# Kernel tuning notes

Measured on AMD Instinct MI355X. Metric: run time of the kernel, lower is better.

The kernel has to match this reference:

```python
import jax, jax.numpy as jnp
import numpy as np

B, L, D = 16, 2048, 128


def setup_inputs() -> dict:
    key = jax.random.key(0)
    k1, k2 = jax.random.split(key)
    x = jax.random.normal(k1, (B, L, D), dtype=jnp.float32)
    mask = jax.random.uniform(k2, (B, L), dtype=jnp.float32)
    return {"input": x, "mask": mask}


def reference(input, mask):
    # mask broadcast over feature dim (torch: mask.unsqueeze(-1).repeat(1,1,D))
    x = input * mask[:, :, None]                       # [B, L, D]
    # attn_weights = bmm(x, x^T) -> [B, L, L]
    scores = jnp.einsum('bld,bmd->blm', x, x)
    # softmax over dim=1 (the FIRST L axis, i.e. columns normalized over rows)
    w = jax.nn.softmax(scores, axis=1)                 # [B, L, L]
    # out = bmm(w^T, x).mean(dim=1, keepdim=True): out_full[b,m,d] = sum_l w[b,l,m] * x[b,l,d]
    out = jnp.einsum('blm,bld->bmd', w, x).mean(axis=1, keepdims=True)  # [B, 1, D]
    attn_mean = w.mean(axis=1)                         # [B, L]
    return (out, attn_mean)
```

## Files before the change

### kernel.cpp

```cpp
#include <hip/hip_runtime.h>
#include <math.h>


constexpr int NB = 16, NL = 2048, ND = 128;
constexpr int ROWS_US = 128;
constexpr int NSLOT = 20;

typedef __attribute__((ext_vector_type(8))) short short8;
typedef __attribute__((ext_vector_type(4))) float f32x4;

#define EXP2(x) __builtin_amdgcn_exp2f(x)

__device__ __forceinline__ unsigned short f2bf(float f) {
  unsigned u = __builtin_bit_cast(unsigned, f);
  u += 0x7FFFu + ((u >> 16) & 1u);
  return (unsigned short)(u >> 16);
}
__device__ __forceinline__ float bf2f(unsigned short h) {
  unsigned u = ((unsigned)h) << 16;
  return __builtin_bit_cast(float, u);
}

__device__ __forceinline__ void stage16(const unsigned short* g, unsigned short* l) {
  __builtin_amdgcn_global_load_lds(
      (const __attribute__((address_space(1))) unsigned int*)g,
      (__attribute__((address_space(3))) unsigned int*)l, 16, 0, 0);
}

__global__ __launch_bounds__(256) void k_prep(const float* __restrict__ x,
                                              const float* __restrict__ mask,
                                              unsigned short* __restrict__ Y,
                                              float* __restrict__ nsq) {
  const int gid = blockIdx.x * 256 + threadIdx.x;
  const int row = gid >> 5;
  const int dq = gid & 31;
  const float4 v = reinterpret_cast<const float4*>(x)[gid];
  const float m = mask[row] * 1.2011224087864498f;
  const unsigned short h0 = f2bf(v.x * m), h1 = f2bf(v.y * m),
                       h2 = f2bf(v.z * m), h3 = f2bf(v.w * m);
  const float g0 = bf2f(h0), g1 = bf2f(h1), g2 = bf2f(h2), g3 = bf2f(h3);
  unsigned short* Yr = Y + (size_t)row * ROWS_US;
  const int sx = dq >> 1, half8 = (dq & 1) * 4;
  const int pos = sx ^ (row & 15);
  *reinterpret_cast<ushort4*>(Yr + pos * 8 + half8) = make_ushort4(h0, h1, h2, h3);
  float ss = g0 * g0 + g1 * g1 + g2 * g2 + g3 * g3;
#pragma unroll
  for (int mk = 1; mk < 32; mk <<= 1) ss += __shfl_xor(ss, mk);
  if (dq == 0) nsq[row] = ss;
}

__global__ __launch_bounds__(256) void k_nmax(const float* __restrict__ nsq,
                                              float* __restrict__ nmax) {
  const int b = blockIdx.x;
  const int tid = threadIdx.x;
  float m = 0.f;
  for (int i = tid; i < NL; i += 256) m = fmaxf(m, nsq[b * NL + i]);
#pragma unroll
  for (int mk = 1; mk < 64; mk <<= 1) m = fmaxf(m, __shfl_xor(m, mk));
  __shared__ float red[4];
  if ((tid & 63) == 0) red[tid >> 6] = m;
  __syncthreads();
  if (tid == 0) nmax[b] = fmaxf(fmaxf(red[0], red[1]), fmaxf(red[2], red[3]));
}

#define STRIP_DECODE()                                     \
  const int sid = blockIdx.x;                              \
  const int idx = sid >> 3;                                \
  const int b = ((sid & 7) << 1) | (idx >> 5);             \
  const int strip = idx & 31;                              \
  const int ib = strip >> 1, hf = strip & 1;               \
  const int d0 = hf * 4;                                   \
  const int nt = (hf == 0) ? 4 : ((ib < 8) ? 5 : 4);       \
  const int row0 = ib * 128;                               \
  const int tid = threadIdx.x;                             \
  const int lane = tid & 63, wave = tid >> 6;              \
  const int wr = wave >> 1, wc = wave & 1;                 \
  const int lhi = lane >> 4, llo = lane & 15;

#define STAGE_AT(dst, Yb, r0)                                               \
  _Pragma("unroll") for (int it = 0; it < 8; ++it) {                        \
    const int idx2 = tid + 256 * it;                                        \
    const int r = idx2 >> 4, s = idx2 & 15;                                 \
    stage16((Yb) + (size_t)((r0) + r) * ROWS_US + s * 8, (dst) + idx2 * 8); \
  }

#define STAGE_BH(dst, Yb, c0)                                               \
  _Pragma("unroll") for (int it = 0; it < 4; ++it) {                        \
    const int idx2 = tid + 256 * it;                                        \
    const int r = idx2 >> 4, s = idx2 & 15;                                 \
    stage16((Yb) + (size_t)((c0) + r) * ROWS_US + s * 8, (dst) + idx2 * 8); \
  }

#define HALF_MFMA(Atp, Btp)                                                  \
  f32x4 acc[4][2];                                                           \
  _Pragma("unroll") for (int rs = 0; rs < 4; ++rs)                           \
      _Pragma("unroll") for (int cs = 0; cs < 2; ++cs)                       \
          acc[rs][cs] = f32x4{0.f, 0.f, 0.f, 0.f};                           \
  _Pragma("unroll") for (int t4 = 0; t4 < 4; ++t4) {                         \
    const int sl = 4 * t4 + lhi;                                             \
    short8 af[4], bf[2];                                                     \
    _Pragma("unroll") for (int qq = 0; qq < 4; ++qq) {                       \
      const int ra = 64 * wr + 16 * qq + llo;                                \
      af[qq] = *(const short8*)((Atp) + ra * 128 + ((sl ^ (ra & 15)) << 3)); \
    }                                                                        \
    _Pragma("unroll") for (int cs = 0; cs < 2; ++cs) {                       \
      const int rb = 32 * wc + 16 * cs + llo;                                \
      bf[cs] = *(const short8*)((Btp) + rb * 128 + ((sl ^ (rb & 15)) << 3)); \
    }                                                                        \
    _Pragma("unroll") for (int rs = 0; rs < 4; ++rs)                         \
        _Pragma("unroll") for (int cs = 0; cs < 2; ++cs)                     \
            acc[rs][cs] = __builtin_amdgcn_mfma_f32_16x16x32_bf16(           \
                af[rs], bf[cs], acc[rs][cs], 0, 0, 0);                       \
  }

__global__ __launch_bounds__(256, 3) void k_esum(const unsigned short* __restrict__ Y,
                                                 const float* __restrict__ nsq,
                                                 const float* __restrict__ nmaxf,
                                                 float* __restrict__ pcs) {
  __shared__ alignas(128) char lds[49152];
  unsigned short* At = (unsigned short*)lds;
  unsigned short* Bt = (unsigned short*)(lds + 32768);
  STRIP_DECODE()
  const unsigned short* Yb = Y + (size_t)b * NL * ROWS_US;
  const float Nmx = nmaxf[b];

  float Cr[16];
#pragma unroll
  for (int rs = 0; rs < 4; ++rs)
#pragma unroll
    for (int rg = 0; rg < 4; ++rg)
      Cr[rs * 4 + rg] = sqrtf(nsq[b * NL + row0 + 64 * wr + 16 * rs + 4 * lhi + rg] * Nmx);

  STAGE_AT(At, Yb, row0)

  float racc[16];
#pragma unroll
  for (int i = 0; i < 16; ++i) racc[i] = 0.f;

  for (int dt = 0; dt < nt; ++dt) {
    const int d = d0 + dt;
    const int col0 = ((ib + d) & 15) * 128;
#pragma unroll
    for (int h = 0; h < 2; ++h) {
      const int colh = col0 + 64 * h;
      __syncthreads();
      STAGE_BH(Bt, Yb, colh)
      float Cc[2];
#pragma unroll
      for (int cs = 0; cs < 2; ++cs)
        Cc[cs] = sqrtf(nsq[b * NL + colh + 32 * wc + 16 * cs + llo] * Nmx);
      __syncthreads();
      HALF_MFMA(At, Bt)
#pragma unroll
      for (int rs = 0; rs < 4; ++rs)
#pragma unroll
        for (int rg = 0; rg < 4; ++rg)
          racc[rs * 4 + rg] += EXP2(acc[rs][0][rg] - Cr[rs * 4 + rg]) +
                               EXP2(acc[rs][1][rg] - Cr[rs * 4 + rg]);
      if (d != 0) {
        float* dst = pcs + ((size_t)(b * NSLOT + 4 + 2 * (d - 1) + wr)) * NL + colh;
#pragma unroll
        for (int cs = 0; cs < 2; ++cs) {
          float u = 0.f;
#pragma unroll
          for (int rs = 0; rs < 4; ++rs)
#pragma unroll
            for (int rg = 0; rg < 4; ++rg) u += EXP2(acc[rs][cs][rg] - Cc[cs]);
          u += __shfl_xor(u, 16);
          u += __shfl_xor(u, 32);
          if (lhi == 0) dst[32 * wc + 16 * cs + llo] = u;
        }
      }
    }
  }
#pragma unroll
  for (int i = 0; i < 16; ++i) {
    float s = racc[i];
#pragma unroll
    for (int mk = 1; mk < 16; mk <<= 1) s += __shfl_xor(s, mk);
    racc[i] = s;
  }
  if (llo == 0) {
    float* dst = pcs + ((size_t)(b * NSLOT + 2 * hf + wc)) * NL + row0;
#pragma unroll
    for (int rs = 0; rs < 4; ++rs)
#pragma unroll
      for (int rg = 0; rg < 4; ++rg)
        dst[64 * wr + 16 * rs + 4 * lhi + rg] = racc[rs * 4 + rg];
  }
}

__global__ __launch_bounds__(256) void k_comb(const float* __restrict__ pcs,
                                              const float* __restrict__ nsq,
                                              const float* __restrict__ nmaxf,
                                              float* __restrict__ Q) {
  const int i = blockIdx.x * 256 + threadIdx.x;
  const int b = i >> 11, row = i & (NL - 1);
  const int o = row >> 7;
  float s = 0.f;
#pragma unroll
  for (int c = 0; c < NSLOT; ++c) {
    if (c >= 18 && o < 8) continue;
    s += pcs[((size_t)(b * NSLOT + c)) * NL + row];
  }
  Q[i] = -sqrtf(nsq[i] * nmaxf[b]) - __log2f(s);
}

__global__ __launch_bounds__(256, 3) void k_r(const unsigned short* __restrict__ Y,
                                              const float* __restrict__ Qa,
                                              float* __restrict__ rp) {
  __shared__ alignas(128) char lds[49152];
  unsigned short* At = (unsigned short*)lds;
  unsigned short* Bt = (unsigned short*)(lds + 32768);
  STRIP_DECODE()
  const unsigned short* Yb = Y + (size_t)b * NL * ROWS_US;

  float Qr[16];
#pragma unroll
  for (int rs = 0; rs < 4; ++rs)
#pragma unroll
    for (int rg = 0; rg < 4; ++rg)
      Qr[rs * 4 + rg] = Qa[b * NL + row0 + 64 * wr + 16 * rs + 4 * lhi + rg];

  STAGE_AT(At, Yb, row0)

  float racc[16];
#pragma unroll
  for (int i = 0; i < 16; ++i) racc[i] = 0.f;

  for (int dt = 0; dt < nt; ++dt) {
    const int d = d0 + dt;
    const int col0 = ((ib + d) & 15) * 128;
#pragma unroll
    for (int h = 0; h < 2; ++h) {
      const int colh = col0 + 64 * h;
      __syncthreads();
      STAGE_BH(Bt, Yb, colh)
      float Qc[2];
#pragma unroll
      for (int cs = 0; cs < 2; ++cs)
        Qc[cs] = Qa[b * NL + colh + 32 * wc + 16 * cs + llo];
      __syncthreads();
      HALF_MFMA(At, Bt)
#pragma unroll
      for (int rs = 0; rs < 4; ++rs)
#pragma unroll
        for (int rg = 0; rg < 4; ++rg)
          racc[rs * 4 + rg] += EXP2(acc[rs][0][rg] + Qc[0]) +
                               EXP2(acc[rs][1][rg] + Qc[1]);
      if (d != 0) {
        float* dst = rp + ((size_t)(b * NSLOT + 4 + 2 * (d - 1) + wr)) * NL + colh;
#pragma unroll
        for (int cs = 0; cs < 2; ++cs) {
          float u = 0.f;
#pragma unroll
          for (int rs = 0; rs < 4; ++rs)
#pragma unroll
            for (int rg = 0; rg < 4; ++rg) u += EXP2(acc[rs][cs][rg] + Qr[rs * 4 + rg]);
          u += __shfl_xor(u, 16);
          u += __shfl_xor(u, 32);
          if (lhi == 0) dst[32 * wc + 16 * cs + llo] = u;
        }
      }
    }
  }
#pragma unroll
  for (int i = 0; i < 16; ++i) {
    float s = racc[i];
#pragma unroll
    for (int mk = 1; mk < 16; mk <<= 1) s += __shfl_xor(s, mk);
    racc[i] = s;
  }
  if (llo == 0) {
    float* dst = rp + ((size_t)(b * NSLOT + 2 * hf + wc)) * NL + row0;
#pragma unroll
    for (int rs = 0; rs < 4; ++rs)
#pragma unroll
      for (int rg = 0; rg < 4; ++rg)
        dst[64 * wr + 16 * rs + 4 * lhi + rg] = racc[rs * 4 + rg];
  }
}

__global__ __launch_bounds__(256) void k_outp(const float* __restrict__ x,
                                              const float* __restrict__ mask,
                                              const float* __restrict__ rp,
                                              float* __restrict__ partial) {
  const int b = blockIdx.y;
  const int seg = blockIdx.x;
  const int tid = threadIdx.x;
  const int l0 = seg * 128;
  __shared__ float w_s[128];
  __shared__ float4 red[8][32];
  if (tid < 128) {
    float s = 0.f;
#pragma unroll
    for (int c = 0; c < NSLOT; ++c) {
      if (c >= 18 && seg < 8) continue;
      s += rp[((size_t)(b * NSLOT + c)) * NL + l0 + tid];
    }
    w_s[tid] = s * mask[b * NL + l0 + tid];
  }
  __syncthreads();
  const int dq = tid & 31;
  const int rg = tid >> 5;
  float4 acc = make_float4(0.f, 0.f, 0.f, 0.f);
#pragma unroll 4
  for (int i = 0; i < 16; ++i) {
    const int l = 8 * i + rg;
    const float w = w_s[l];
    const float4 v = *reinterpret_cast<const float4*>(x + ((size_t)b * NL + l0 + l) * ND + 4 * dq);
    acc.x += w * v.x; acc.y += w * v.y; acc.z += w * v.z; acc.w += w * v.w;
  }
  red[rg][dq] = acc;
  __syncthreads();
  if (rg == 0) {
    float4 s = acc;
#pragma unroll
    for (int k = 1; k < 8; ++k) {
      const float4 t = red[k][dq];
      s.x += t.x; s.y += t.y; s.z += t.z; s.w += t.w;
    }
    *reinterpret_cast<float4*>(partial + ((size_t)(b * 16 + seg)) * ND + 4 * dq) = s;
  }
}

__global__ __launch_bounds__(1024) void k_fin(const float* __restrict__ partial,
                                              float* __restrict__ out) {
  const int gid = blockIdx.x * 1024 + threadIdx.x;
  if (gid < NB * ND) {
    const int b = gid >> 7, d = gid & (ND - 1);
    float s = 0.f;
#pragma unroll
    for (int k = 0; k < 16; ++k) s += partial[(size_t)(b * 16 + k) * ND + d];
    out[gid] = s * (1.0f / NL);
  }
  out[NB * ND + gid] = 1.0f / NL;
}

extern "C" void kernel_launch(void* const* d_in, const int* in_sizes, int n_in,
                              void* d_out, int out_size, void* d_ws, size_t ws_size,
                              hipStream_t stream) {
  const float* x = (const float*)d_in[0];
  const float* mask = (const float*)d_in[1];
  float* out = (float*)d_out;

  unsigned short* Y = (unsigned short*)d_ws;
  float* nsq = (float*)(Y + (size_t)NB * NL * ROWS_US);
  float* nmaxf = nsq + NB * NL;
  float* pcs = nmaxf + 16;
  float* rp = pcs;
  float* Q = pcs + (size_t)NB * NSLOT * NL;
  float* partial = Q + NB * NL;

  k_prep<<<dim3(NB * NL * ND / 4 / 256), 256, 0, stream>>>(x, mask, Y, nsq);
  k_nmax<<<NB, 256, 0, stream>>>(nsq, nmaxf);
  k_esum<<<dim3(512), 256, 0, stream>>>(Y, nsq, nmaxf, pcs);
  k_comb<<<dim3(NB * NL / 256), 256, 0, stream>>>(pcs, nsq, nmaxf, Q);
  k_r<<<dim3(512), 256, 0, stream>>>(Y, Q, rp);
  k_outp<<<dim3(16, NB), 256, 0, stream>>>(x, mask, rp, partial);
  k_fin<<<32, 1024, 0, stream>>>(partial, out);
}
```

Measured before the change: 69.59 us.

## Use 512-thread blocks staging full 128-column tiles per step

The two MFMA kernels move from 256 threads covering a 128x64 tile to 512 threads (eight waves in a 2x4 layout) covering a full 128x128 tile per step. This halves the barrier and staging rounds per diagonal tile and raises the number of waves per block. Partial-sum slot counts grow from 20 to 24, so the combine and output kernels read more slots. LDS per block grows to 64KB, which may reduce how many blocks fit on each CU.

```diff
diff --git a/kernel.cpp b/kernel.cpp
--- a/kernel.cpp
+++ b/kernel.cpp
@@ -4,7 +4,7 @@
 
 constexpr int NB = 16, NL = 2048, ND = 128;
 constexpr int ROWS_US = 128;
-constexpr int NSLOT = 20;
+constexpr int NSLOT = 24;
 
 typedef __attribute__((ext_vector_type(8))) short short8;
 typedef __attribute__((ext_vector_type(4))) float f32x4;
@@ -74,24 +74,17 @@
   const int row0 = ib * 128;                               \
   const int tid = threadIdx.x;                             \
   const int lane = tid & 63, wave = tid >> 6;              \
-  const int wr = wave >> 1, wc = wave & 1;                 \
+  const int wr = wave >> 2, wc = wave & 3;                 \
   const int lhi = lane >> 4, llo = lane & 15;
 
-#define STAGE_AT(dst, Yb, r0)                                               \
-  _Pragma("unroll") for (int it = 0; it < 8; ++it) {                        \
-    const int idx2 = tid + 256 * it;                                        \
+#define STAGE_T(dst, Yb, r0)                                                \
+  _Pragma("unroll") for (int it = 0; it < 4; ++it) {                        \
+    const int idx2 = tid + 512 * it;                                        \
     const int r = idx2 >> 4, s = idx2 & 15;                                 \
     stage16((Yb) + (size_t)((r0) + r) * ROWS_US + s * 8, (dst) + idx2 * 8); \
   }
 
-#define STAGE_BH(dst, Yb, c0)                                               \
-  _Pragma("unroll") for (int it = 0; it < 4; ++it) {                        \
-    const int idx2 = tid + 256 * it;                                        \
-    const int r = idx2 >> 4, s = idx2 & 15;                                 \
-    stage16((Yb) + (size_t)((c0) + r) * ROWS_US + s * 8, (dst) + idx2 * 8); \
-  }
-
-#define HALF_MFMA(Atp, Btp)                                                  \
+#define TILE_MFMA(Atp, Btp)                                                  \
   f32x4 acc[4][2];                                                           \
   _Pragma("unroll") for (int rs = 0; rs < 4; ++rs)                           \
       _Pragma("unroll") for (int cs = 0; cs < 2; ++cs)                       \
@@ -113,11 +106,11 @@
                 af[rs], bf[cs], acc[rs][cs], 0, 0, 0);                       \
   }
 
-__global__ __launch_bounds__(256, 3) void k_esum(const unsigned short* __restrict__ Y,
+__global__ __launch_bounds__(512, 4) void k_esum(const unsigned short* __restrict__ Y,
                                                  const float* __restrict__ nsq,
                                                  const float* __restrict__ nmaxf,
                                                  float* __restrict__ pcs) {
-  __shared__ alignas(128) char lds[49152];
+  __shared__ alignas(128) char lds[65536];
   unsigned short* At = (unsigned short*)lds;
   unsigned short* Bt = (unsigned short*)(lds + 32768);
   STRIP_DECODE()
@@ -131,7 +124,7 @@
     for (int rg = 0; rg < 4; ++rg)
       Cr[rs * 4 + rg] = sqrtf(nsq[b * NL + row0 + 64 * wr + 16 * rs + 4 * lhi + rg] * Nmx);
 
-  STAGE_AT(At, Yb, row0)
+  STAGE_T(At, Yb, row0)
 
   float racc[16];
 #pragma unroll
@@ -140,36 +133,32 @@
   for (int dt = 0; dt < nt; ++dt) {
     const int d = d0 + dt;
     const int col0 = ((ib + d) & 15) * 128;
-#pragma unroll
-    for (int h = 0; h < 2; ++h) {
-      const int colh = col0 + 64 * h;
-      __syncthreads();
-      STAGE_BH(Bt, Yb, colh)
-      float Cc[2];
-#pragma unroll
-      for (int cs = 0; cs < 2; ++cs)
-        Cc[cs] = sqrtf(nsq[b * NL + colh + 32 * wc + 16 * cs + llo] * Nmx);
-      __syncthreads();
-      HALF_MFMA(At, Bt)
-#pragma unroll
-      for (int rs = 0; rs < 4; ++rs)
-#pragma unroll
-        for (int rg = 0; rg < 4; ++rg)
-          racc[rs * 4 + rg] += EXP2(acc[rs][0][rg] - Cr[rs * 4 + rg]) +
-                               EXP2(acc[rs][1][rg] - Cr[rs * 4 + rg]);
-      if (d != 0) {
-        float* dst = pcs + ((size_t)(b * NSLOT + 4 + 2 * (d - 1) + wr)) * NL + colh;
-#pragma unroll
-        for (int cs = 0; cs < 2; ++cs) {
-          float u = 0.f;
-#pragma unroll
-          for (int rs = 0; rs < 4; ++rs)
-#pragma unroll
-            for (int rg = 0; rg < 4; ++rg) u += EXP2(acc[rs][cs][rg] - Cc[cs]);
-          u += __shfl_xor(u, 16);
-          u += __shfl_xor(u, 32);
-          if (lhi == 0) dst[32 * wc + 16 * cs + llo] = u;
-        }
+    __syncthreads();
+    STAGE_T(Bt, Yb, col0)
+    float Cc[2];
+#pragma unroll
+    for (int cs = 0; cs < 2; ++cs)
+      Cc[cs] = sqrtf(nsq[b * NL + col0 + 32 * wc + 16 * cs + llo] * Nmx);
+    __syncthreads();
+    TILE_MFMA(At, Bt)
+#pragma unroll
+    for (int rs = 0; rs < 4; ++rs)
+#pragma unroll
+      for (int rg = 0; rg < 4; ++rg)
+        racc[rs * 4 + rg] += EXP2(acc[rs][0][rg] - Cr[rs * 4 + rg]) +
+                             EXP2(acc[rs][1][rg] - Cr[rs * 4 + rg]);
+    if (d != 0) {
+      float* dst = pcs + ((size_t)(b * NSLOT + 8 + 2 * (d - 1) + wr)) * NL + col0;
+#pragma unroll
+      for (int cs = 0; cs < 2; ++cs) {
+        float u = 0.f;
+#pragma unroll
+        for (int rs = 0; rs < 4; ++rs)
+#pragma unroll
+          for (int rg = 0; rg < 4; ++rg) u += EXP2(acc[rs][cs][rg] - Cc[cs]);
+        u += __shfl_xor(u, 16);
+        u += __shfl_xor(u, 32);
+        if (lhi == 0) dst[32 * wc + 16 * cs + llo] = u;
       }
     }
   }
@@ -181,7 +170,7 @@
     racc[i] = s;
   }
   if (llo == 0) {
-    float* dst = pcs + ((size_t)(b * NSLOT + 2 * hf + wc)) * NL + row0;
+    float* dst = pcs + ((size_t)(b * NSLOT + 4 * hf + wc)) * NL + row0;
 #pragma unroll
     for (int rs = 0; rs < 4; ++rs)
 #pragma unroll
@@ -200,16 +189,16 @@
   float s = 0.f;
 #pragma unroll
   for (int c = 0; c < NSLOT; ++c) {
-    if (c >= 18 && o < 8) continue;
+    if (c >= 22 && o < 8) continue;
     s += pcs[((size_t)(b * NSLOT + c)) * NL + row];
   }
   Q[i] = -sqrtf(nsq[i] * nmaxf[b]) - __log2f(s);
 }
 
-__global__ __launch_bounds__(256, 3) void k_r(const unsigned short* __restrict__ Y,
+__global__ __launch_bounds__(512, 4) void k_r(const unsigned short* __restrict__ Y,
                                               const float* __restrict__ Qa,
                                               float* __restrict__ rp) {
-  __shared__ alignas(128) char lds[49152];
+  __shared__ alignas(128) char lds[65536];
   unsigned short* At = (unsigned short*)lds;
   unsigned short* Bt = (unsigned short*)(lds + 32768);
   STRIP_DECODE()
@@ -222,7 +211,7 @@
     for (int rg = 0; rg < 4; ++rg)
       Qr[rs * 4 + rg] = Qa[b * NL + row0 + 64 * wr + 16 * rs + 4 * lhi + rg];
 
-  STAGE_AT(At, Yb, row0)
+  STAGE_T(At, Yb, row0)
 
   float racc[16];
 #pragma unroll
@@ -231,36 +220,32 @@
   for (int dt = 0; dt < nt; ++dt) {
     const int d = d0 + dt;
     const int col0 = ((ib + d) & 15) * 128;
-#pragma unroll
-    for (int h = 0; h < 2; ++h) {
-      const int colh = col0 + 64 * h;
-      __syncthreads();
-      STAGE_BH(Bt, Yb, colh)
-      float Qc[2];
-#pragma unroll
-      for (int cs = 0; cs < 2; ++cs)
-        Qc[cs] = Qa[b * NL + colh + 32 * wc + 16 * cs + llo];
-      __syncthreads();
-      HALF_MFMA(At, Bt)
-#pragma unroll
-      for (int rs = 0; rs < 4; ++rs)
-#pragma unroll
-        for (int rg = 0; rg < 4; ++rg)
-          racc[rs * 4 + rg] += EXP2(acc[rs][0][rg] + Qc[0]) +
-                               EXP2(acc[rs][1][rg] + Qc[1]);
-      if (d != 0) {
-        float* dst = rp + ((size_t)(b * NSLOT + 4 + 2 * (d - 1) + wr)) * NL + colh;
-#pragma unroll
-        for (int cs = 0; cs < 2; ++cs) {
-          float u = 0.f;
-#pragma unroll
-          for (int rs = 0; rs < 4; ++rs)
-#pragma unroll
-            for (int rg = 0; rg < 4; ++rg) u += EXP2(acc[rs][cs][rg] + Qr[rs * 4 + rg]);
-          u += __shfl_xor(u, 16);
-          u += __shfl_xor(u, 32);
-          if (lhi == 0) dst[32 * wc + 16 * cs + llo] = u;
-        }
+    __syncthreads();
+    STAGE_T(Bt, Yb, col0)
+    float Qc[2];
+#pragma unroll
+    for (int cs = 0; cs < 2; ++cs)
+      Qc[cs] = Qa[b * NL + col0 + 32 * wc + 16 * cs + llo];
+    __syncthreads();
+    TILE_MFMA(At, Bt)
+#pragma unroll
+    for (int rs = 0; rs < 4; ++rs)
+#pragma unroll
+      for (int rg = 0; rg < 4; ++rg)
+        racc[rs * 4 + rg] += EXP2(acc[rs][0][rg] + Qc[0]) +
+                             EXP2(acc[rs][1][rg] + Qc[1]);
+    if (d != 0) {
+      float* dst = rp + ((size_t)(b * NSLOT + 8 + 2 * (d - 1) + wr)) * NL + col0;
+#pragma unroll
+      for (int cs = 0; cs < 2; ++cs) {
+        float u = 0.f;
+#pragma unroll
+        for (int rs = 0; rs < 4; ++rs)
+#pragma unroll
+          for (int rg = 0; rg < 4; ++rg) u += EXP2(acc[rs][cs][rg] + Qr[rs * 4 + rg]);
+        u += __shfl_xor(u, 16);
+        u += __shfl_xor(u, 32);
+        if (lhi == 0) dst[32 * wc + 16 * cs + llo] = u;
       }
     }
   }
@@ -272,7 +257,7 @@
     racc[i] = s;
   }
   if (llo == 0) {
-    float* dst = rp + ((size_t)(b * NSLOT + 2 * hf + wc)) * NL + row0;
+    float* dst = rp + ((size_t)(b * NSLOT + 4 * hf + wc)) * NL + row0;
 #pragma unroll
     for (int rs = 0; rs < 4; ++rs)
 #pragma unroll
@@ -295,7 +280,7 @@
     float s = 0.f;
 #pragma unroll
     for (int c = 0; c < NSLOT; ++c) {
-      if (c >= 18 && seg < 8) continue;
+      if (c >= 22 && seg < 8) continue;
       s += rp[((size_t)(b * NSLOT + c)) * NL + l0 + tid];
     }
     w_s[tid] = s * mask[b * NL + l0 + tid];
@@ -354,9 +339,9 @@
 
   k_prep<<<dim3(NB * NL * ND / 4 / 256), 256, 0, stream>>>(x, mask, Y, nsq);
   k_nmax<<<NB, 256, 0, stream>>>(nsq, nmaxf);
-  k_esum<<<dim3(512), 256, 0, stream>>>(Y, nsq, nmaxf, pcs);
+  k_esum<<<dim3(512), 512, 0, stream>>>(Y, nsq, nmaxf, pcs);
   k_comb<<<dim3(NB * NL / 256), 256, 0, stream>>>(pcs, nsq, nmaxf, Q);
-  k_r<<<dim3(512), 256, 0, stream>>>(Y, Q, rp);
+  k_r<<<dim3(512), 512, 0, stream>>>(Y, Q, rp);
   k_outp<<<dim3(16, NB), 256, 0, stream>>>(x, mask, rp, partial);
   k_fin<<<32, 1024, 0, stream>>>(partial, out);
 }
```

Result: faster. 66.10 us (-5.0%).
